# Performance work log

Measured on AMD Instinct MI355X. Metric: run time of the kernel, lower is better.

The kernel has to match this reference:

```python
import jax, jax.numpy as jnp
from jax import lax
import numpy as np

T, B, D = 24, 64, 1536
R, NUM_BLOCK = 5120, 5
NBN = R // NUM_BLOCK  # 1024 neurons per block
C = 100
THR_BASE = 0.5
REF_BASE = 0.5
Q0 = 0.8  # (100-20)/100 from wta_mem_update


@jax.custom_vjp
def spike_fn(v):
    # act_fun: heaviside forward, rectangular surrogate gradient
    return (v > 0).astype(v.dtype)

def _spike_fwd(v):
    return (v > 0).astype(v.dtype), v

def _spike_bwd(v, g):
    return (g * (jnp.abs(v) < 0.5).astype(g.dtype),)

spike_fn.defvjp(_spike_fwd, _spike_bwd)


def setup_inputs() -> dict:
    key = jax.random.key(0)
    ks = jax.random.split(key, 16)
    f32 = jnp.float32
    x = jax.random.normal(ks[0], (T, B, D), dtype=f32)
    Wp = jax.random.normal(ks[1], (R, D), dtype=f32) / np.sqrt(D)
    Wl = jax.random.normal(ks[2], (R, R), dtype=f32) / np.sqrt(R)
    Wm = jax.random.normal(ks[3], (C, R), dtype=f32) / np.sqrt(R)
    # adaptive LIF per-neuron parameters (as in __init__)
    decay = jax.random.uniform(ks[4], (R,), dtype=f32)
    thr_beta = 0.1 * jax.random.uniform(ks[5], (R,), dtype=f32)
    thr_decay = 0.5 * jax.random.uniform(ks[6], (R,), dtype=f32)
    ref_beta = 0.1 * jax.random.uniform(ks[7], (R,), dtype=f32)
    ref_decay = 0.5 * jax.random.uniform(ks[8], (R,), dtype=f32)
    cur_beta = 0.1 * jax.random.uniform(ks[9], (R,), dtype=f32)
    cur_decay = 0.5 * jax.random.uniform(ks[10], (R,), dtype=f32)
    # block-structured projection mask: [D, R] then transpose to weight layout [R, D]
    mask = np.zeros((D, R), dtype=np.float32)
    cum = np.cumsum([0, 512, 512, 256, 128])  # [0,512,1024,1280,1408]
    for i in range(len(cum) - 1):
        mask[cum[i]:cum[i + 1], NBN * i:NBN * (i + 1)] = 1.0
    proj_mask = jnp.asarray(mask.T)
    # sparse lateral mask: rand>0.8, no self-connection
    rng = np.random.RandomState(0)
    lat = (rng.rand(R, R) > 0.8).astype(np.float32)
    lat = lat * (1.0 - np.eye(R, dtype=np.float32))
    lat_mask = jnp.asarray(lat.T)
    return {
        "x": x, "ln_g": jnp.ones((D,), f32), "ln_b": jnp.zeros((D,), f32),
        "Wp": Wp, "bp": jnp.zeros((R,), f32), "Wl": Wl, "bl": jnp.zeros((R,), f32),
        "Wm": Wm, "bm": jnp.zeros((C,), f32),
        "decay": decay, "thr_beta": thr_beta, "thr_decay": thr_decay,
        "ref_beta": ref_beta, "ref_decay": ref_decay,
        "cur_beta": cur_beta, "cur_decay": cur_decay,
        "proj_mask": proj_mask, "lat_mask": lat_mask,
    }


def reference(x, ln_g, ln_b, Wp, bp, Wl, bl, Wm, bm,
              decay, thr_beta, thr_decay, ref_beta, ref_decay,
              cur_beta, cur_decay, proj_mask, lat_mask):
    Tn, Bn, Dn = x.shape
    Rn = Wp.shape[0]
    # parameter clamps done in forward of the torch module
    dec = jnp.clip(decay, 0.0, 1.0)
    thd = jnp.clip(thr_decay, 0.0, 1.0)
    rfd = jnp.clip(ref_decay, 0.0, 1.0)
    cud = jnp.clip(cur_decay, 0.0, 1.0)
    Wp_m = Wp * proj_mask       # masked feedforward projection
    Wl_m = Wl * lat_mask        # masked lateral recurrence
    # LayerNorm over fused multimodal features
    mu = x.mean(-1, keepdims=True)
    var = x.var(-1, keepdims=True)
    xn = (x - mu) * lax.rsqrt(var + 1e-5) * ln_g + ln_b
    # precompute feedforward drive for all steps: [T, B, R]
    drive = jnp.einsum('tbd,rd->tbr', xn, Wp_m) + bp

    def step(carry, dr_t):
        spike, mem, ttr, rtr, ctr, ssum = carry
        state = dr_t + spike @ Wl_m.T + bl
        thr = THR_BASE + thr_beta * ttr
        ref = REF_BASE + ref_beta * rtr
        cur = cur_beta * ctr
        mem = (mem - spike * ref) * dec + state + cur
        # WTA: quantile-threshold per group (torch row-major reshape [B, NBN, NUM_BLOCK])
        m3 = mem.reshape(Bn, NBN, NUM_BLOCK)
        nps = jnp.quantile(m3, Q0, axis=1, keepdims=True)
        mem = jax.nn.relu(m3 - nps).reshape(Bn, Rn)
        spk = spike_fn(mem - thr)
        ttr = ttr * thd + spk
        rtr = rtr * rfd + spk
        ctr = ctr * cud + spk
        return (spk, mem, ttr, rtr, ctr, ssum + spk), None

    z = jnp.zeros((Bn, Rn), x.dtype)
    (spk, mem, _, _, _, ssum), _ = lax.scan(step, (z, z, z, z, z, z), drive)
    # readout on time-averaged spike counts
    return (ssum / Tn) @ Wm.T + bm
```

## Files before the change

### kernel.cpp

```cpp
#include <hip/hip_runtime.h>
#include <math.h>

#define TSTEPS 24
#define BB 64
#define DD 1536
#define RR 5120
#define NB 5
#define CC 100
#define KS 2
#define WSCALE 67108864.0

typedef int i32x4 __attribute__((ext_vector_type(4)));

__device__ __forceinline__ int q_to_r(int q) { return (q & 1023) * 5 + (q >> 10); }

__constant__ int KOFF[4] = {0, 512, 1024, 1280};
__constant__ int KLEN[4] = {512, 512, 256, 128};
__constant__ int PBASE[4] = {0, 524288, 1048576, 1310720};

__device__ __forceinline__ unsigned fkey(float f) {
  unsigned u = __float_as_uint(f);
  return u ^ (((unsigned)((int)u >> 31)) | 0x80000000u);
}
__device__ __forceinline__ float fkeyinv(unsigned k) {
  unsigned u = (k & 0x80000000u) ? (k ^ 0x80000000u) : ~k;
  return __uint_as_float(u);
}

__global__ __launch_bounds__(256) void k_zero(float* __restrict__ state,
                                              unsigned* __restrict__ spike_i8_u32) {
  size_t n = 6ull * BB * RR;
  size_t nb = (size_t)BB * RR / 4;
  size_t gi = (size_t)blockIdx.x * 256 + threadIdx.x;
  for (size_t i = gi; i < n; i += (size_t)gridDim.x * 256) state[i] = 0.0f;
  for (size_t i = gi; i < nb; i += (size_t)gridDim.x * 256) spike_i8_u32[i] = 0u;
}

__global__ __launch_bounds__(256) void k_prep_params(
    const float* __restrict__ bp, const float* __restrict__ bl,
    const float* __restrict__ dec, const float* __restrict__ tb,
    const float* __restrict__ td, const float* __restrict__ rb,
    const float* __restrict__ rd, const float* __restrict__ cb,
    const float* __restrict__ cd, float* __restrict__ P) {
  int q = blockIdx.x * 256 + threadIdx.x;
  if (q >= RR) return;
  int r = q_to_r(q);
  P[0 * RR + q] = bp[r] + bl[r];
  P[1 * RR + q] = fminf(fmaxf(dec[r], 0.f), 1.f);
  P[2 * RR + q] = tb[r];
  P[3 * RR + q] = fminf(fmaxf(td[r], 0.f), 1.f);
  P[4 * RR + q] = rb[r];
  P[5 * RR + q] = fminf(fmaxf(rd[r], 0.f), 1.f);
  P[6 * RR + q] = cb[r];
  P[7 * RR + q] = fminf(fmaxf(cd[r], 0.f), 1.f);
}

__global__ __launch_bounds__(256) void k_prep_wm(const float* __restrict__ Wm,
                                                 float* __restrict__ Wmp) {
  int c = blockIdx.x;
  for (int q = threadIdx.x; q < RR; q += 256)
    Wmp[(size_t)c * RR + q] = Wm[(size_t)c * RR + q_to_r(q)];
}

__global__ __launch_bounds__(256) void k_prep_wpb(const float* __restrict__ Wp,
                                                  const float* __restrict__ pm,
                                                  float* __restrict__ Wpb) {
  int r = blockIdx.x;
  int i = r >> 10;
  int koff = KOFF[i], klen = KLEN[i];
  const float* src = Wp + (size_t)r * DD + koff;
  const float* msk = pm + (size_t)r * DD + koff;
  float* dst = Wpb + PBASE[i] + (size_t)(r - (i << 10)) * klen;
  for (int k = threadIdx.x; k < klen; k += 256) dst[k] = src[k] * msk[k];
}

__global__ __launch_bounds__(256) void k_build_q4tab(const float* __restrict__ bp,
                                                     const float* __restrict__ bl,
                                                     int* __restrict__ qtab,
                                                     float* __restrict__ vtab) {
  for (int idx = threadIdx.x; idx < 1024; idx += 256) {
    int j, i;
    if (idx < 204) { j = 0; i = 820 + idx; }
    else { int e = idx - 204; j = 1 + e / 205; i = 819 + e % 205; }
    int r = i * 5 + j;
    qtab[idx] = j * 1024 + i;
    vtab[idx] = bp[r] + bl[r];
  }
}

__global__ __launch_bounds__(256) void k_build_wq_i8(const float* __restrict__ Wl,
                                                     const float* __restrict__ lmask,
                                                     signed char* __restrict__ Bd) {
  int qn = blockIdx.x;
  int rn = q_to_r(qn);
  const float* wr = Wl + (size_t)rn * RR;
  const float* mr = lmask + (size_t)rn * RR;
  size_t ob = (size_t)qn * RR;
  const size_t plane = (size_t)RR * RR;
  for (int rk = threadIdx.x; rk < RR; rk += 256) {
    float w = wr[rk] * mr[rk];
    long long wi = llrint((double)w * WSCALE);
    int d0 = (int)(signed char)(wi & 0xFF);
    long long rem = (wi - d0) >> 8;
    int d1 = (int)(signed char)(rem & 0xFF);
    rem = (rem - d1) >> 8;
    Bd[ob + rk] = (signed char)d0;
    Bd[plane + ob + rk] = (signed char)d1;
    Bd[2 * plane + ob + rk] = (signed char)rem;
  }
}

__global__ __launch_bounds__(256) void k_layernorm(const float* __restrict__ x,
                                                   const float* __restrict__ g,
                                                   const float* __restrict__ be,
                                                   float* __restrict__ xn) {
  __shared__ float red[4];
  int row = blockIdx.x;
  int tid = threadIdx.x;
  const float* xr = x + (size_t)row * DD;
  float v[6];
  float s = 0.f;
#pragma unroll
  for (int i = 0; i < 6; i++) { v[i] = xr[i * 256 + tid]; s += v[i]; }
  for (int o = 32; o > 0; o >>= 1) s += __shfl_down(s, o, 64);
  int wv = tid >> 6, lane = tid & 63;
  if (lane == 0) red[wv] = s;
  __syncthreads();
  float mu = (red[0] + red[1] + red[2] + red[3]) * (1.0f / DD);
  __syncthreads();
  float sq = 0.f;
#pragma unroll
  for (int i = 0; i < 6; i++) { float d = v[i] - mu; sq += d * d; }
  for (int o = 32; o > 0; o >>= 1) sq += __shfl_down(sq, o, 64);
  if (lane == 0) red[wv] = sq;
  __syncthreads();
  float var = (red[0] + red[1] + red[2] + red[3]) * (1.0f / DD);
  float sc = 1.0f / sqrtf(var + 1e-5f);
#pragma unroll
  for (int i = 0; i < 6; i++) {
    int c = i * 256 + tid;
    xn[(size_t)row * DD + c] = (v[i] - mu) * sc * g[c] + be[c];
  }
}

__global__ __launch_bounds__(256) void k_gemm_drive(const float* __restrict__ A,
                                                    const float* __restrict__ Wpb,
                                                    const float* __restrict__ bp,
                                                    const float* __restrict__ bl,
                                                    float* __restrict__ Co) {
  __shared__ __align__(16) float As[16][68];
  __shared__ __align__(16) float Bs[16][68];
  int tid = threadIdx.x;
  int ib = blockIdx.z;
  int klen = KLEN[ib], koff = KOFF[ib];
  int m0 = blockIdx.y * 64;
  int n0t = blockIdx.x * 64;
  int lr = tid >> 2;
  int lq = tid & 3;
  int tx = tid & 15;
  int ty = tid >> 4;
  float acc[4][4] = {};
  const float4* Arow = (const float4*)(A + (size_t)(m0 + lr) * DD + koff);
  const float4* Brow = (const float4*)(Wpb + PBASE[ib] + (size_t)(n0t + lr) * klen);
  for (int k0 = 0; k0 < klen; k0 += 16) {
    float4 av = Arow[(k0 >> 2) + lq];
    float4 bv = Brow[(k0 >> 2) + lq];
    __syncthreads();
    As[lq * 4 + 0][lr] = av.x; As[lq * 4 + 1][lr] = av.y;
    As[lq * 4 + 2][lr] = av.z; As[lq * 4 + 3][lr] = av.w;
    Bs[lq * 4 + 0][lr] = bv.x; Bs[lq * 4 + 1][lr] = bv.y;
    Bs[lq * 4 + 2][lr] = bv.z; Bs[lq * 4 + 3][lr] = bv.w;
    __syncthreads();
#pragma unroll
    for (int kk = 0; kk < 16; kk++) {
      float4 a4 = *(const float4*)&As[kk][ty * 4];
      float4 b4 = *(const float4*)&Bs[kk][tx * 4];
      float av2[4] = {a4.x, a4.y, a4.z, a4.w};
      float bv2[4] = {b4.x, b4.y, b4.z, b4.w};
#pragma unroll
      for (int i2 = 0; i2 < 4; i2++)
#pragma unroll
        for (int j2 = 0; j2 < 4; j2++) acc[i2][j2] += av2[i2] * bv2[j2];
    }
  }
  int rbase = (ib << 10) + n0t + tx * 4;
  float bb[4];
  int qd[4];
#pragma unroll
  for (int j2 = 0; j2 < 4; j2++) {
    int rr = rbase + j2;
    bb[j2] = bp[rr] + bl[rr];
    qd[j2] = (rr % 5) * 1024 + rr / 5;
  }
#pragma unroll
  for (int i2 = 0; i2 < 4; i2++) {
    float* orow = Co + (size_t)(m0 + ty * 4 + i2) * RR;
#pragma unroll
    for (int j2 = 0; j2 < 4; j2++) orow[qd[j2]] = acc[i2][j2] + bb[j2];
  }
}

__global__ __launch_bounds__(256) void k_drive_fill4(const int* __restrict__ qtab,
                                                     const float* __restrict__ vtab,
                                                     float* __restrict__ drive) {
  int row = blockIdx.x;
  float* dr = drive + (size_t)row * RR;
  for (int k = threadIdx.x; k < 1024; k += 256) dr[qtab[k]] = vtab[k];
}

__global__ __launch_bounds__(256) void k_lat_gemm(const signed char* __restrict__ Asp,
                                                  const signed char* __restrict__ Bd,
                                                  long long* __restrict__ latp) {
  __shared__ long long lds[4][16][64];
  int tid = threadIdx.x;
  int lane = tid & 63;
  int w = tid >> 6;
  int n0 = blockIdx.x * 16;
  int ks = blockIdx.y;
  int k0 = ks * (RR / KS) + w * (RR / (KS * 4));
  int lm = lane & 15, lh = lane >> 4;
  const size_t plane = (size_t)RR * RR;
  i32x4 acc[4][3];
#pragma unroll
  for (int s = 0; s < 4; s++)
#pragma unroll
    for (int d = 0; d < 3; d++) acc[s][d] = (i32x4){0, 0, 0, 0};
  const i32x4* ap0 = (const i32x4*)(Asp + (size_t)(lm) * RR + k0 + lh * 16);
  const i32x4* ap1 = (const i32x4*)(Asp + (size_t)(16 + lm) * RR + k0 + lh * 16);
  const i32x4* ap2 = (const i32x4*)(Asp + (size_t)(32 + lm) * RR + k0 + lh * 16);
  const i32x4* ap3 = (const i32x4*)(Asp + (size_t)(48 + lm) * RR + k0 + lh * 16);
  const i32x4* bp0 = (const i32x4*)(Bd + (size_t)(n0 + lm) * RR + k0 + lh * 16);
  const i32x4* bp1 = (const i32x4*)(Bd + plane + (size_t)(n0 + lm) * RR + k0 + lh * 16);
  const i32x4* bp2 = (const i32x4*)(Bd + 2 * plane + (size_t)(n0 + lm) * RR + k0 + lh * 16);
#pragma unroll 2
  for (int kk = 0; kk < RR / (KS * 4 * 64); kk++) {
    i32x4 a0 = ap0[kk * 4];
    i32x4 a1 = ap1[kk * 4];
    i32x4 a2 = ap2[kk * 4];
    i32x4 a3 = ap3[kk * 4];
    i32x4 b0 = bp0[kk * 4];
    i32x4 b1 = bp1[kk * 4];
    i32x4 b2 = bp2[kk * 4];
    acc[0][0] = __builtin_amdgcn_mfma_i32_16x16x64_i8(a0, b0, acc[0][0], 0, 0, 0);
    acc[1][0] = __builtin_amdgcn_mfma_i32_16x16x64_i8(a1, b0, acc[1][0], 0, 0, 0);
    acc[2][0] = __builtin_amdgcn_mfma_i32_16x16x64_i8(a2, b0, acc[2][0], 0, 0, 0);
    acc[3][0] = __builtin_amdgcn_mfma_i32_16x16x64_i8(a3, b0, acc[3][0], 0, 0, 0);
    acc[0][1] = __builtin_amdgcn_mfma_i32_16x16x64_i8(a0, b1, acc[0][1], 0, 0, 0);
    acc[1][1] = __builtin_amdgcn_mfma_i32_16x16x64_i8(a1, b1, acc[1][1], 0, 0, 0);
    acc[2][1] = __builtin_amdgcn_mfma_i32_16x16x64_i8(a2, b1, acc[2][1], 0, 0, 0);
    acc[3][1] = __builtin_amdgcn_mfma_i32_16x16x64_i8(a3, b1, acc[3][1], 0, 0, 0);
    acc[0][2] = __builtin_amdgcn_mfma_i32_16x16x64_i8(a0, b2, acc[0][2], 0, 0, 0);
    acc[1][2] = __builtin_amdgcn_mfma_i32_16x16x64_i8(a1, b2, acc[1][2], 0, 0, 0);
    acc[2][2] = __builtin_amdgcn_mfma_i32_16x16x64_i8(a2, b2, acc[2][2], 0, 0, 0);
    acc[3][2] = __builtin_amdgcn_mfma_i32_16x16x64_i8(a3, b2, acc[3][2], 0, 0, 0);
  }
#pragma unroll
  for (int s = 0; s < 4; s++) {
#pragma unroll
    for (int r = 0; r < 4; r++) {
      long long v = (long long)acc[s][0][r]
                  + ((long long)acc[s][1][r] << 8)
                  + ((long long)acc[s][2][r] << 16);
      lds[w][s * 4 + r][lane] = v;
    }
  }
  __syncthreads();
  int o0 = tid * 4;
  int m = o0 >> 4;
  int ncb = o0 & 15;
  int s = m >> 4, lh2 = (m >> 2) & 3, rr = m & 3;
  long long* ob = latp + (size_t)ks * BB * RR + (size_t)m * RR + n0;
#pragma unroll
  for (int u = 0; u < 4; u++) {
    int nc = ncb + u;
    long long v = lds[0][s * 4 + rr][lh2 * 16 + nc]
                + lds[1][s * 4 + rr][lh2 * 16 + nc]
                + lds[2][s * 4 + rr][lh2 * 16 + nc]
                + lds[3][s * 4 + rr][lh2 * 16 + nc];
    ob[nc] = v;
  }
}

__global__ __launch_bounds__(256) void k_step(
    const float* __restrict__ drv_t,
    const long long* __restrict__ latp,
    const float* __restrict__ P,
    float* __restrict__ spike, float* __restrict__ memv,
    float* __restrict__ ttr, float* __restrict__ rtr, float* __restrict__ ctr,
    float* __restrict__ ssum, unsigned char* __restrict__ spike_i8) {
  __shared__ unsigned hist[256];
  __shared__ unsigned wtot[4];
  __shared__ unsigned s_prefix, s_rank, s_cle, s_min;

  int tid = threadIdx.x;
  int lane = tid & 63;
  int wv = tid >> 6;
  int j = blockIdx.x;
  int b = blockIdx.y;
  if (tid == 0) { s_prefix = 0u; s_rank = 818u; s_cle = 0u; s_min = 0xFFFFFFFFu; }

  size_t pbase4 = (size_t)b * RR + j * 1024 + 4 * tid;
  long long li[4] = {0, 0, 0, 0};
#pragma unroll
  for (int ks = 0; ks < KS; ks++) {
    const long long* p = latp + (size_t)ks * BB * RR + pbase4;
    li[0] += p[0]; li[1] += p[1]; li[2] += p[2]; li[3] += p[3];
  }
  float acc[4];
#pragma unroll
  for (int c = 0; c < 4; c++) acc[c] = (float)((double)li[c] * (1.0 / WSCALE));

  size_t sbase = pbase4;
  int pbase = j * 1024 + 4 * tid;
  float4 drv4 = *(const float4*)(drv_t + sbase);
  float4 mem4 = *(const float4*)(memv + sbase);
  float4 sp4 = *(const float4*)(spike + sbase);
  float4 tt4 = *(const float4*)(ttr + sbase);
  float4 tr4 = *(const float4*)(rtr + sbase);
  float4 tc4 = *(const float4*)(ctr + sbase);
  float4 dec4 = *(const float4*)(P + 1 * RR + pbase);
  float4 tb4 = *(const float4*)(P + 2 * RR + pbase);
  float4 rb4 = *(const float4*)(P + 4 * RR + pbase);
  float4 cb4 = *(const float4*)(P + 6 * RR + pbase);
  float mn[4], th[4];
  {
    const float* dv = (const float*)&drv4;
    const float* mv = (const float*)&mem4;
    const float* sv = (const float*)&sp4;
    const float* t1 = (const float*)&tt4;
    const float* t2 = (const float*)&tr4;
    const float* t3 = (const float*)&tc4;
    const float* dc = (const float*)&dec4;
    const float* b1 = (const float*)&tb4;
    const float* b2 = (const float*)&rb4;
    const float* b3 = (const float*)&cb4;
#pragma unroll
    for (int c = 0; c < 4; c++) {
      float rf = 0.5f + b2[c] * t2[c];
      float cu = b3[c] * t3[c];
      th[c] = 0.5f + b1[c] * t1[c];
      mn[c] = (mv[c] - sv[c] * rf) * dc[c] + (dv[c] + acc[c]) + cu;
    }
  }
  unsigned k4[4];
#pragma unroll
  for (int c = 0; c < 4; c++) k4[c] = fkey(mn[c]);

#pragma unroll
  for (int pass = 0; pass < 4; pass++) {
    int shift = 24 - pass * 8;
    unsigned maskhi = (pass == 0) ? 0u : (0xFFFFFFFFu << (shift + 8));
    hist[tid] = 0u;
    __syncthreads();
    unsigned pfx = s_prefix;
    unsigned rank = s_rank;
#pragma unroll
    for (int c = 0; c < 4; c++)
      if ((k4[c] & maskhi) == (pfx & maskhi)) atomicAdd(&hist[(k4[c] >> shift) & 255u], 1u);
    __syncthreads();
    unsigned cnt0 = hist[tid];
    unsigned v = cnt0;
    for (int o = 1; o < 64; o <<= 1) {
      unsigned n = (unsigned)__shfl_up((int)v, o, 64);
      if (lane >= o) v += n;
    }
    if (lane == 63) wtot[wv] = v;
    __syncthreads();
    unsigned add = 0;
    for (int w = 0; w < wv; w++) add += wtot[w];
    unsigned incl = v + add;
    unsigned excl = incl - cnt0;
    if (rank >= excl && rank < incl) {
      s_prefix = pfx | (((unsigned)tid) << shift);
      s_rank = rank - excl;
    }
    __syncthreads();
  }
  unsigned u818 = s_prefix;
  {
    int cl = 0;
    unsigned mnk = 0xFFFFFFFFu;
#pragma unroll
    for (int c = 0; c < 4; c++) {
      cl += (k4[c] <= u818) ? 1 : 0;
      if (k4[c] > u818) mnk = min(mnk, k4[c]);
    }
    atomicAdd(&s_cle, (unsigned)cl);
    atomicMin(&s_min, mnk);
  }
  __syncthreads();
  unsigned u819 = (s_cle >= 820u) ? u818 : s_min;
  float f818 = fkeyinv(u818), f819 = fkeyinv(u819);
  float nps = f818 + (0.8f * 1023.0f - 818.0f) * (f819 - f818);

  float4 td4 = *(const float4*)(P + 3 * RR + pbase);
  float4 rd4 = *(const float4*)(P + 5 * RR + pbase);
  float4 cd4 = *(const float4*)(P + 7 * RR + pbase);
  float4 ss4 = *(const float4*)(ssum + sbase);
  unsigned char si[4];
  {
    const float* d1 = (const float*)&td4;
    const float* d2 = (const float*)&rd4;
    const float* d3 = (const float*)&cd4;
    float* t1 = (float*)&tt4;
    float* t2 = (float*)&tr4;
    float* t3 = (float*)&tc4;
    float* sv = (float*)&sp4;
    float* mv = (float*)&mem4;
    float* ss = (float*)&ss4;
#pragma unroll
    for (int c = 0; c < 4; c++) {
      float mw = fmaxf(mn[c] - nps, 0.f);
      float sk = (mw - th[c] > 0.f) ? 1.f : 0.f;
      si[c] = (sk > 0.5f) ? (unsigned char)1 : (unsigned char)0;
      mv[c] = mw;
      t1[c] = t1[c] * d1[c] + sk;
      t2[c] = t2[c] * d2[c] + sk;
      t3[c] = t3[c] * d3[c] + sk;
      sv[c] = sk;
      ss[c] += sk;
    }
  }
  *(float4*)(memv + sbase) = mem4;
  *(float4*)(spike + sbase) = sp4;
  *(float4*)(ttr + sbase) = tt4;
  *(float4*)(rtr + sbase) = tr4;
  *(float4*)(ctr + sbase) = tc4;
  *(float4*)(ssum + sbase) = ss4;
  {
    unsigned char* sb8 = spike_i8 + (size_t)b * RR;
    int ibase = 4 * tid;
#pragma unroll
    for (int c = 0; c < 4; c++) sb8[(ibase + c) * 5 + j] = si[c];
  }
}

__global__ __launch_bounds__(256) void k_readout(const float* __restrict__ ssum,
                                                 const float* __restrict__ Wmp,
                                                 const float* __restrict__ bm,
                                                 float* __restrict__ out) {
  __shared__ float red[4];
  int c = blockIdx.x;
  int b = blockIdx.y;
  int tid = threadIdx.x;
  const float4* sp = (const float4*)(ssum + (size_t)b * RR);
  const float4* wp = (const float4*)(Wmp + (size_t)c * RR);
  float acc = 0.f;
#pragma unroll
  for (int i = 0; i < 5; i++) {
    float4 s4 = sp[i * 256 + tid];
    float4 w4 = wp[i * 256 + tid];
    acc += s4.x * w4.x + s4.y * w4.y + s4.z * w4.z + s4.w * w4.w;
  }
  for (int o = 32; o > 0; o >>= 1) acc += __shfl_down(acc, o, 64);
  if ((tid & 63) == 0) red[tid >> 6] = acc;
  __syncthreads();
  if (tid == 0)
    out[b * CC + c] = (red[0] + red[1] + red[2] + red[3]) * (1.0f / 24.0f) + bm[c];
}

extern "C" void kernel_launch(void* const* d_in, const int* in_sizes, int n_in,
                              void* d_out, int out_size, void* d_ws, size_t ws_size,
                              hipStream_t stream) {
  const float* x = (const float*)d_in[0];
  const float* ln_g = (const float*)d_in[1];
  const float* ln_b = (const float*)d_in[2];
  const float* Wp = (const float*)d_in[3];
  const float* bp = (const float*)d_in[4];
  const float* Wl = (const float*)d_in[5];
  const float* bl = (const float*)d_in[6];
  const float* Wm = (const float*)d_in[7];
  const float* bm = (const float*)d_in[8];
  const float* decay = (const float*)d_in[9];
  const float* thr_beta = (const float*)d_in[10];
  const float* thr_decay = (const float*)d_in[11];
  const float* ref_beta = (const float*)d_in[12];
  const float* ref_decay = (const float*)d_in[13];
  const float* cur_beta = (const float*)d_in[14];
  const float* cur_decay = (const float*)d_in[15];
  const float* proj_mask = (const float*)d_in[16];
  const float* lat_mask = (const float*)d_in[17];
  float* out = (float*)d_out;

  float* ws = (float*)d_ws;
  float* Wpb = ws;
  float* xn = Wpb + 1442 * 1024;
  float* drive = xn + (size_t)TSTEPS * BB * DD;
  float* state = drive + (size_t)TSTEPS * BB * RR;
  float* spike = state;
  float* memv = spike + (size_t)BB * RR;
  float* ttr = memv + (size_t)BB * RR;
  float* rtr = ttr + (size_t)BB * RR;
  float* ctr = rtr + (size_t)BB * RR;
  float* ssum = ctr + (size_t)BB * RR;
  float* P = ssum + (size_t)BB * RR;
  float* Wmp = P + 8 * RR;
  int* qtab = (int*)(Wmp + (size_t)CC * RR);
  float* vtab = (float*)(qtab + 1024);
  long long* latp = (long long*)(vtab + 1024 + 64);
  signed char* Bd = (signed char*)(latp + (size_t)KS * BB * RR);
  unsigned char* spike_i8 = (unsigned char*)(Bd + 3ull * RR * RR);

  hipLaunchKernelGGL(k_zero, dim3(512), dim3(256), 0, stream, state,
                     (unsigned*)spike_i8);
  hipLaunchKernelGGL(k_prep_params, dim3((RR + 255) / 256), dim3(256), 0, stream,
                     bp, bl, decay, thr_beta, thr_decay, ref_beta, ref_decay,
                     cur_beta, cur_decay, P);
  hipLaunchKernelGGL(k_prep_wm, dim3(CC), dim3(256), 0, stream, Wm, Wmp);
  hipLaunchKernelGGL(k_prep_wpb, dim3(4096), dim3(256), 0, stream, Wp, proj_mask, Wpb);
  hipLaunchKernelGGL(k_build_q4tab, dim3(1), dim3(256), 0, stream, bp, bl, qtab, vtab);
  hipLaunchKernelGGL(k_build_wq_i8, dim3(RR), dim3(256), 0, stream, Wl, lat_mask, Bd);
  hipLaunchKernelGGL(k_layernorm, dim3(TSTEPS * BB), dim3(256), 0, stream,
                     x, ln_g, ln_b, xn);
  hipLaunchKernelGGL(k_gemm_drive, dim3(16, (TSTEPS * BB) / 64, 4), dim3(256), 0,
                     stream, xn, Wpb, bp, bl, drive);
  hipLaunchKernelGGL(k_drive_fill4, dim3(TSTEPS * BB), dim3(256), 0, stream,
                     qtab, vtab, drive);
  for (int t = 0; t < TSTEPS; t++) {
    hipLaunchKernelGGL(k_lat_gemm, dim3(RR / 16, KS), dim3(256), 0, stream,
                       (const signed char*)spike_i8, Bd, latp);
    hipLaunchKernelGGL(k_step, dim3(NB, BB), dim3(256), 0, stream,
                       drive + (size_t)t * BB * RR, latp, P,
                       spike, memv, ttr, rtr, ctr, ssum, spike_i8);
  }
  hipLaunchKernelGGL(k_readout, dim3(CC, BB), dim3(256), 0, stream, ssum, Wmp, bm, out);
}
```

Baseline: 1.152 ms.

## Drop split-K in lateral GEMM, emit float output, vectorize weight quantization

The lateral int8 GEMM no longer splits K across two grid slices. Each block now reduces the full K range across its four waves and writes scaled float results directly, so the step kernel reads one float4 instead of summing two int64 partials. The weight-quantization prep kernel is vectorized with float4 loads and uchar4 stores and uses float rintf instead of double llrint. The trade-off is half as many GEMM blocks (320), which lowers parallelism per timestep, and float rounding in the quantization could differ slightly from the double path.

```diff
diff --git a/kernel.cpp b/kernel.cpp
--- a/kernel.cpp
+++ b/kernel.cpp
@@ -7,8 +7,7 @@
 #define RR 5120
 #define NB 5
 #define CC 100
-#define KS 2
-#define WSCALE 67108864.0
+#define WSCALE 67108864.0f
 
 typedef int i32x4 __attribute__((ext_vector_type(4)));
 
@@ -93,20 +92,29 @@
                                                      signed char* __restrict__ Bd) {
   int qn = blockIdx.x;
   int rn = q_to_r(qn);
-  const float* wr = Wl + (size_t)rn * RR;
-  const float* mr = lmask + (size_t)rn * RR;
+  const float4* wr = (const float4*)(Wl + (size_t)rn * RR);
+  const float4* mr = (const float4*)(lmask + (size_t)rn * RR);
   size_t ob = (size_t)qn * RR;
   const size_t plane = (size_t)RR * RR;
-  for (int rk = threadIdx.x; rk < RR; rk += 256) {
-    float w = wr[rk] * mr[rk];
-    long long wi = llrint((double)w * WSCALE);
-    int d0 = (int)(signed char)(wi & 0xFF);
-    long long rem = (wi - d0) >> 8;
-    int d1 = (int)(signed char)(rem & 0xFF);
-    rem = (rem - d1) >> 8;
-    Bd[ob + rk] = (signed char)d0;
-    Bd[plane + ob + rk] = (signed char)d1;
-    Bd[2 * plane + ob + rk] = (signed char)rem;
+  for (int v4 = threadIdx.x; v4 < RR / 4; v4 += 256) {
+    float4 wv = wr[v4];
+    float4 mv = mr[v4];
+    float w[4] = {wv.x * mv.x, wv.y * mv.y, wv.z * mv.z, wv.w * mv.w};
+    unsigned char o0[4], o1[4], o2[4];
+#pragma unroll
+    for (int c = 0; c < 4; c++) {
+      int wi = (int)rintf(w[c] * WSCALE);
+      int d0 = (int)(signed char)(wi & 0xFF);
+      int rem = (wi - d0) >> 8;
+      int d1 = (int)(signed char)(rem & 0xFF);
+      rem = (rem - d1) >> 8;
+      o0[c] = (unsigned char)d0;
+      o1[c] = (unsigned char)d1;
+      o2[c] = (unsigned char)(rem & 0xFF);
+    }
+    *(uchar4*)(Bd + ob + 4 * v4) = make_uchar4(o0[0], o0[1], o0[2], o0[3]);
+    *(uchar4*)(Bd + plane + ob + 4 * v4) = make_uchar4(o1[0], o1[1], o1[2], o1[3]);
+    *(uchar4*)(Bd + 2 * plane + ob + 4 * v4) = make_uchar4(o2[0], o2[1], o2[2], o2[3]);
   }
 }
 
@@ -210,14 +218,13 @@
 
 __global__ __launch_bounds__(256) void k_lat_gemm(const signed char* __restrict__ Asp,
                                                   const signed char* __restrict__ Bd,
-                                                  long long* __restrict__ latp) {
+                                                  float* __restrict__ latf) {
   __shared__ long long lds[4][16][64];
   int tid = threadIdx.x;
   int lane = tid & 63;
   int w = tid >> 6;
   int n0 = blockIdx.x * 16;
-  int ks = blockIdx.y;
-  int k0 = ks * (RR / KS) + w * (RR / (KS * 4));
+  int k0 = w * 1280;
   int lm = lane & 15, lh = lane >> 4;
   const size_t plane = (size_t)RR * RR;
   i32x4 acc[4][3];
@@ -233,7 +240,7 @@
   const i32x4* bp1 = (const i32x4*)(Bd + plane + (size_t)(n0 + lm) * RR + k0 + lh * 16);
   const i32x4* bp2 = (const i32x4*)(Bd + 2 * plane + (size_t)(n0 + lm) * RR + k0 + lh * 16);
 #pragma unroll 2
-  for (int kk = 0; kk < RR / (KS * 4 * 64); kk++) {
+  for (int kk = 0; kk < 20; kk++) {
     i32x4 a0 = ap0[kk * 4];
     i32x4 a1 = ap1[kk * 4];
     i32x4 a2 = ap2[kk * 4];
@@ -269,7 +276,7 @@
   int m = o0 >> 4;
   int ncb = o0 & 15;
   int s = m >> 4, lh2 = (m >> 2) & 3, rr = m & 3;
-  long long* ob = latp + (size_t)ks * BB * RR + (size_t)m * RR + n0;
+  float* ob = latf + (size_t)m * RR + n0;
 #pragma unroll
   for (int u = 0; u < 4; u++) {
     int nc = ncb + u;
@@ -277,13 +284,13 @@
                 + lds[1][s * 4 + rr][lh2 * 16 + nc]
                 + lds[2][s * 4 + rr][lh2 * 16 + nc]
                 + lds[3][s * 4 + rr][lh2 * 16 + nc];
-    ob[nc] = v;
+    ob[nc] = (float)((double)v * (1.0 / (double)WSCALE));
   }
 }
 
 __global__ __launch_bounds__(256) void k_step(
     const float* __restrict__ drv_t,
-    const long long* __restrict__ latp,
+    const float* __restrict__ latf,
     const float* __restrict__ P,
     float* __restrict__ spike, float* __restrict__ memv,
     float* __restrict__ ttr, float* __restrict__ rtr, float* __restrict__ ctr,
@@ -299,19 +306,9 @@
   int b = blockIdx.y;
   if (tid == 0) { s_prefix = 0u; s_rank = 818u; s_cle = 0u; s_min = 0xFFFFFFFFu; }
 
-  size_t pbase4 = (size_t)b * RR + j * 1024 + 4 * tid;
-  long long li[4] = {0, 0, 0, 0};
-#pragma unroll
-  for (int ks = 0; ks < KS; ks++) {
-    const long long* p = latp + (size_t)ks * BB * RR + pbase4;
-    li[0] += p[0]; li[1] += p[1]; li[2] += p[2]; li[3] += p[3];
-  }
-  float acc[4];
-#pragma unroll
-  for (int c = 0; c < 4; c++) acc[c] = (float)((double)li[c] * (1.0 / WSCALE));
-
-  size_t sbase = pbase4;
+  size_t sbase = (size_t)b * RR + j * 1024 + 4 * tid;
   int pbase = j * 1024 + 4 * tid;
+  float4 lat4 = *(const float4*)(latf + sbase);
   float4 drv4 = *(const float4*)(drv_t + sbase);
   float4 mem4 = *(const float4*)(memv + sbase);
   float4 sp4 = *(const float4*)(spike + sbase);
@@ -324,6 +321,7 @@
   float4 cb4 = *(const float4*)(P + 6 * RR + pbase);
   float mn[4], th[4];
   {
+    const float* av = (const float*)&lat4;
     const float* dv = (const float*)&drv4;
     const float* mv = (const float*)&mem4;
     const float* sv = (const float*)&sp4;
@@ -339,7 +337,7 @@
       float rf = 0.5f + b2[c] * t2[c];
       float cu = b3[c] * t3[c];
       th[c] = 0.5f + b1[c] * t1[c];
-      mn[c] = (mv[c] - sv[c] * rf) * dc[c] + (dv[c] + acc[c]) + cu;
+      mn[c] = (mv[c] - sv[c] * rf) * dc[c] + (dv[c] + av[c]) + cu;
     }
   }
   unsigned k4[4];
@@ -497,8 +495,8 @@
   float* Wmp = P + 8 * RR;
   int* qtab = (int*)(Wmp + (size_t)CC * RR);
   float* vtab = (float*)(qtab + 1024);
-  long long* latp = (long long*)(vtab + 1024 + 64);
-  signed char* Bd = (signed char*)(latp + (size_t)KS * BB * RR);
+  float* latf = vtab + 1024 + 64;
+  signed char* Bd = (signed char*)(latf + (size_t)BB * RR);
   unsigned char* spike_i8 = (unsigned char*)(Bd + 3ull * RR * RR);
 
   hipLaunchKernelGGL(k_zero, dim3(512), dim3(256), 0, stream, state,
@@ -517,10 +515,10 @@
   hipLaunchKernelGGL(k_drive_fill4, dim3(TSTEPS * BB), dim3(256), 0, stream,
                      qtab, vtab, drive);
   for (int t = 0; t < TSTEPS; t++) {
-    hipLaunchKernelGGL(k_lat_gemm, dim3(RR / 16, KS), dim3(256), 0, stream,
-                       (const signed char*)spike_i8, Bd, latp);
+    hipLaunchKernelGGL(k_lat_gemm, dim3(RR / 16), dim3(256), 0, stream,
+                       (const signed char*)spike_i8, Bd, latf);
     hipLaunchKernelGGL(k_step, dim3(NB, BB), dim3(256), 0, stream,
-                       drive + (size_t)t * BB * RR, latp, P,
+                       drive + (size_t)t * BB * RR, latf, P,
                        spike, memv, ttr, rtr, ctr, ssum, spike_i8);
   }
   hipLaunchKernelGGL(k_readout, dim3(CC, BB), dim3(256), 0, stream, ssum, Wmp, bm, out);
```

Measured after the change: 1.285 ms. 11.5% more time.
